# Kernel tuning notes

Hardware: AMD Instinct MI355X
Metric: run time of the kernel (lower is better)

The kernel has to match this reference:

```python
import jax, jax.numpy as jnp
import numpy as np

N_USERS = 100000
N_ITEMS = 50000
N_NODES = N_USERS + N_ITEMS
NNZ = 2400000
EMB_DIM = 64
N_LAYERS = 3
BATCH = 16384
REG = 1e-5


def setup_inputs() -> dict:
    key = jax.random.key(0)
    ks = jax.random.split(key, 12)
    return {
        "adj_row": jax.random.randint(ks[0], (NNZ,), 0, N_NODES, dtype=jnp.int32),
        "adj_col": jax.random.randint(ks[1], (NNZ,), 0, N_NODES, dtype=jnp.int32),
        "adj_val": jax.random.uniform(ks[2], (NNZ,), dtype=jnp.float32),
        "user_emb": jax.random.normal(ks[3], (N_USERS, EMB_DIM), dtype=jnp.float32) * 0.1,
        "item_emb": jax.random.normal(ks[4], (N_ITEMS, EMB_DIM), dtype=jnp.float32) * 0.1,
        "W1": jax.random.normal(ks[5], (N_LAYERS, EMB_DIM, EMB_DIM), dtype=jnp.float32) * 0.1,
        "b1": jax.random.normal(ks[6], (N_LAYERS, EMB_DIM), dtype=jnp.float32) * 0.1,
        "W2": jax.random.normal(ks[7], (N_LAYERS, EMB_DIM, EMB_DIM), dtype=jnp.float32) * 0.1,
        "b2": jax.random.normal(ks[8], (N_LAYERS, EMB_DIM), dtype=jnp.float32) * 0.1,
        "u": jax.random.randint(ks[9], (BATCH,), 0, N_USERS, dtype=jnp.int32),
        "i": jax.random.randint(ks[10], (BATCH,), 0, N_ITEMS, dtype=jnp.int32),
        "j": jax.random.randint(ks[11], (BATCH,), 0, N_ITEMS, dtype=jnp.int32),
    }


def _spmm(row, col, val, x):
    # sparse.mm(L, x): gather source rows, scale by edge value, scatter-add to dest
    msgs = val[:, None] * x[col]  # [nnz, d]
    return jax.ops.segment_sum(msgs, row, num_segments=N_NODES)


def reference(adj_row, adj_col, adj_val, user_emb, item_emb, W1, b1, W2, b2, u, i, j):
    ego = jnp.concatenate([user_emb, item_emb], axis=0)  # [N, d]
    finals = [ego]
    for k in range(N_LAYERS):
        side_L = _spmm(adj_row, adj_col, adj_val, ego)      # L @ ego
        side_LI = side_L + ego                               # (L + I) @ ego
        simple = side_LI @ W1[k] + b1[k]
        inter = (ego * side_L) @ W2[k] + b2[k]
        ego = jax.nn.leaky_relu(simple + inter, negative_slope=0.01)
        # mess_dropout = 0 -> identity; F.normalize(p=2, dim=1, eps=1e-12)
        nrm = jnp.linalg.norm(ego, axis=1, keepdims=True)
        finals.append(ego / jnp.maximum(nrm, 1e-12))
    final = jnp.concatenate(finals, axis=1)  # [N, d*(L+1)]
    u_f, i_f = final[:N_USERS], final[N_USERS:]
    u_emb = u_f[u]
    p_emb = i_f[i]
    n_emb = i_f[j]
    y_ui = jnp.sum(u_emb * p_emb, axis=1)
    y_uj = jnp.sum(u_emb * n_emb, axis=1)
    bpr_loss = -jnp.mean(jax.nn.log_sigmoid(y_ui - y_uj))
    l2norm = (jnp.sum(u_emb ** 2) / 2.0 + jnp.sum(p_emb ** 2) / 2.0 + jnp.sum(n_emb ** 2) / 2.0) / u_emb.shape[0]
    return bpr_loss + REG * l2norm
```

## Files before the change

kernel.cpp:

```cpp
#include <hip/hip_runtime.h>

#define N_USERS 100000
#define N_ITEMS 50000
#define N_NODES 150000
#define NNZ     2400000
#define EMB     64
#define NLAYERS 3
#define BATCH   16384
#define REG     1e-5f

#define NTILES ((N_NODES + 63) / 64)

#define ROWS_PER_BUCKET 256
#define NB_BUCKET ((N_NODES + ROWS_PER_BUCKET - 1) / ROWS_PER_BUCKET)
#define BIN_CHUNK 8192
#define BIN_NB ((NNZ + BIN_CHUNK - 1) / BIN_CHUNK)
#define BCAP 6144

#define F8_SCALE 16.0f
#define F8_INV   0.0625f

typedef __attribute__((ext_vector_type(8))) short bfrag8;
typedef __attribute__((ext_vector_type(4))) float vf4;
typedef __attribute__((ext_vector_type(2))) float f32x2;


__device__ inline unsigned short f2bf(float x) {
    unsigned int u = __builtin_bit_cast(unsigned int, x);
    return (unsigned short)((u + 0x7fffu + ((u >> 16) & 1u)) >> 16);
}
__device__ inline float bf2f(unsigned short h) {
    unsigned int u = ((unsigned int)h) << 16;
    return __builtin_bit_cast(float, u);
}

__global__ __launch_bounds__(256) void init_ego_kernel(
    const float* __restrict__ ue, const float* __restrict__ ie,
    unsigned short* __restrict__ ego_bf, unsigned char* __restrict__ ego_f8) {
    int idx = blockIdx.x * 256 + threadIdx.x;
    if (idx >= N_NODES * 16) return;
    int row = idx >> 4, q = idx & 15;
    const float* src = (row < N_USERS)
                           ? ue + (size_t)row * 64
                           : ie + (size_t)(row - N_USERS) * 64;
    float v0 = src[q], v1 = src[16 + q], v2 = src[32 + q], v3 = src[48 + q];
    uint2 o;
    o.x = (unsigned)f2bf(v0) | ((unsigned)f2bf(v1) << 16);
    o.y = (unsigned)f2bf(v2) | ((unsigned)f2bf(v3) << 16);
    ((uint2*)ego_bf)[(size_t)row * 16 + q] = o;
    int u = __builtin_amdgcn_cvt_pk_fp8_f32(v0 * F8_SCALE, v1 * F8_SCALE, 0,
                                            false);
    u = __builtin_amdgcn_cvt_pk_fp8_f32(v2 * F8_SCALE, v3 * F8_SCALE, u, true);
    ((int*)ego_f8)[(size_t)row * 16 + q] = u;
}

__global__ __launch_bounds__(256) void prep_w_kernel(
    const float* __restrict__ W1, const float* __restrict__ W2,
    unsigned short* __restrict__ BT) {
    int idx = blockIdx.x * blockDim.x + threadIdx.x;
    if (idx >= NLAYERS * 64 * 128) return;
    int l = idx / 8192;
    int rem = idx - l * 8192;
    int j = rem >> 7;
    int k = rem & 127;
    int p = k & 63;
    int d = ((p & 3) << 4) | (p >> 2);
    float w = (k < 64) ? W1[l * 4096 + d * 64 + j]
                       : W2[l * 4096 + d * 64 + j];
    BT[idx] = f2bf(w);
}

__global__ __launch_bounds__(1024) void binscatter_kernel(
    const int* __restrict__ row, const int* __restrict__ col,
    const float* __restrict__ val, int* __restrict__ bcnt,
    int2* __restrict__ stage) {
    __shared__ int hist[NB_BUCKET];
    __shared__ int wbase[NB_BUCKET];
    const int t = threadIdx.x;
    const int s = blockIdx.x * BIN_CHUNK;
    const int e = min(s + BIN_CHUNK, NNZ);

    for (int b = t; b < NB_BUCKET; b += 1024) hist[b] = 0;
    __syncthreads();
    for (int i = s + t; i < e; i += 1024)
        atomicAdd(&hist[row[i] >> 8], 1);
    __syncthreads();
    for (int b = t; b < NB_BUCKET; b += 1024) {
        int c = hist[b];
        wbase[b] = c ? atomicAdd(&bcnt[b], c) : 0;
        hist[b] = 0;
    }
    __syncthreads();
    for (int i0 = s + t; i0 < e; i0 += 4096) {
        int i1 = i0 + 1024, i2 = i0 + 2048, i3 = i0 + 3072;
        bool v1 = i1 < e, v2 = i2 < e, v3 = i3 < e;
        int r0 = row[i0];
        int r1 = v1 ? row[i1] : 0;
        int r2 = v2 ? row[i2] : 0;
        int r3 = v3 ? row[i3] : 0;
        int c0 = col[i0];
        int c1 = v1 ? col[i1] : 0;
        int c2 = v2 ? col[i2] : 0;
        int c3 = v3 ? col[i3] : 0;
        float w0 = val[i0];
        float w1 = v1 ? val[i1] : 0.f;
        float w2 = v2 ? val[i2] : 0.f;
        float w3 = v3 ? val[i3] : 0.f;
        int b0 = r0 >> 8, b1 = r1 >> 8, b2 = r2 >> 8, b3 = r3 >> 8;
        int o0 = atomicAdd(&hist[b0], 1);
        int o1 = v1 ? atomicAdd(&hist[b1], 1) : 0;
        int o2 = v2 ? atomicAdd(&hist[b2], 1) : 0;
        int o3 = v3 ? atomicAdd(&hist[b3], 1) : 0;
        stage[(size_t)b0 * BCAP + wbase[b0] + o0] =
            make_int2(c0 | ((r0 & 255) << 18), __builtin_bit_cast(int, w0));
        if (v1)
            stage[(size_t)b1 * BCAP + wbase[b1] + o1] =
                make_int2(c1 | ((r1 & 255) << 18), __builtin_bit_cast(int, w1));
        if (v2)
            stage[(size_t)b2 * BCAP + wbase[b2] + o2] =
                make_int2(c2 | ((r2 & 255) << 18), __builtin_bit_cast(int, w2));
        if (v3)
            stage[(size_t)b3 * BCAP + wbase[b3] + o3] =
                make_int2(c3 | ((r3 & 255) << 18), __builtin_bit_cast(int, w3));
    }
}

__global__ __launch_bounds__(1024) void bscan_kernel(
    const int* __restrict__ bcnt, int* __restrict__ bbase) {
    __shared__ int sc[1024];
    const int t = threadIdx.x;
    int v = (t < NB_BUCKET) ? bcnt[t] : 0;
    sc[t] = v;
    __syncthreads();
    int x = v;
    for (int off = 1; off < 1024; off <<= 1) {
        int y = (t >= off) ? sc[t - off] : 0;
        __syncthreads();
        x += y;
        sc[t] = x;
        __syncthreads();
    }
    if (t < NB_BUCKET) bbase[t] = x - v;
    if (t == 0) bbase[NB_BUCKET] = NNZ;
}

__global__ __launch_bounds__(1024) void bucket_place_kernel(
    const int2* __restrict__ stage, const int* __restrict__ bcnt,
    const int* __restrict__ bbase, int* __restrict__ rp,
    int2* __restrict__ sce) {
    __shared__ int cnt[ROWS_PER_BUCKET];
    __shared__ int sc[ROWS_PER_BUCKET];
    __shared__ int cur[ROWS_PER_BUCKET];
    const int b = blockIdx.x;
    const int t = threadIdx.x;
    const int row0 = b * ROWS_PER_BUCKET;
    const size_t S0 = (size_t)b * BCAP;
    const int ne = bcnt[b];
    const int B0 = bbase[b];
    if (t < 256) cnt[t] = 0;
    __syncthreads();
    for (int i = t; i < ne; i += 1024)
        atomicAdd(&cnt[(stage[S0 + i].x >> 18) & 255], 1);
    __syncthreads();
    int v = 0, x = 0;
    if (t < 256) { v = cnt[t]; x = v; sc[t] = v; }
    __syncthreads();
    for (int off = 1; off < 256; off <<= 1) {
        int y = (t < 256 && t >= off) ? sc[t - off] : 0;
        __syncthreads();
        if (t < 256) { x += y; sc[t] = x; }
        __syncthreads();
    }
    if (t < 256) {
        int excl = x - v;
        int row = row0 + t;
        if (row <= N_NODES) rp[row] = B0 + excl;
        cur[t] = B0 + excl;
    }
    __syncthreads();
    for (int i = t; i < ne; i += 1024) {
        int2 pk = stage[S0 + i];
        int rl = (pk.x >> 18) & 255;
        int pos = atomicAdd(&cur[rl], 1);
        sce[pos] = make_int2(pk.x & 0x3FFFF, pk.y);
    }
}

__global__ __launch_bounds__(256) void spmm_csr_kernel(
    const int* __restrict__ rp, const int2* __restrict__ sce,
    const unsigned char* __restrict__ ego_f8,
    unsigned short* __restrict__ side_bf) {
    const int lane = threadIdx.x & 63;
    const int q    = lane >> 4;
    const int ql   = lane & 15;
    int w = (blockIdx.x * blockDim.x + threadIdx.x) >> 6;
    int r0 = 2 * w;
    if (r0 >= N_NODES) return;
    int r1 = r0 + 1;
    const bool has1 = (r1 < N_NODES);
    const int* egoF = (const int*)ego_f8;
    int s0 = rp[r0];
    int e0 = rp[r0 + 1];
    int s1 = e0;
    int e1 = has1 ? rp[r0 + 2] : e0;
    float A0 = 0.f, A1 = 0.f, A2 = 0.f, A3 = 0.f;
    float B0 = 0.f, B1 = 0.f, B2 = 0.f, B3 = 0.f;

#define F8A(gi, wi)                                                          \
    {                                                                        \
        f32x2 lo_ = __builtin_amdgcn_cvt_pk_f32_fp8(gi, false);              \
        f32x2 hi_ = __builtin_amdgcn_cvt_pk_f32_fp8(gi, true);               \
        A0 = fmaf(wi, lo_.x, A0);                                            \
        A1 = fmaf(wi, lo_.y, A1);                                            \
        A2 = fmaf(wi, hi_.x, A2);                                            \
        A3 = fmaf(wi, hi_.y, A3);                                            \
    }
#define F8B(gi, wi)                                                          \
    {                                                                        \
        f32x2 lo_ = __builtin_amdgcn_cvt_pk_f32_fp8(gi, false);              \
        f32x2 hi_ = __builtin_amdgcn_cvt_pk_f32_fp8(gi, true);               \
        B0 = fmaf(wi, lo_.x, B0);                                            \
        B1 = fmaf(wi, lo_.y, B1);                                            \
        B2 = fmaf(wi, hi_.x, B2);                                            \
        B3 = fmaf(wi, hi_.y, B3);                                            \
    }

    int k0 = s0, k1 = s1;
    while (k0 + 15 < e0 || k1 + 15 < e1) {
        bool d0 = (k0 + 15 < e0), d1 = (k1 + 15 < e1);
        int2 cA0, cA1, cA2, cA3, cB0, cB1, cB2, cB3;
        int gA0 = 0, gA1 = 0, gA2 = 0, gA3 = 0;
        int gB0 = 0, gB1 = 0, gB2 = 0, gB3 = 0;
        if (d0) {
            cA0 = sce[k0 + q];      cA1 = sce[k0 + 4 + q];
            cA2 = sce[k0 + 8 + q];  cA3 = sce[k0 + 12 + q];
        }
        if (d1) {
            cB0 = sce[k1 + q];      cB1 = sce[k1 + 4 + q];
            cB2 = sce[k1 + 8 + q];  cB3 = sce[k1 + 12 + q];
        }
        if (d0) {
            gA0 = egoF[(size_t)cA0.x * 16 + ql];
            gA1 = egoF[(size_t)cA1.x * 16 + ql];
            gA2 = egoF[(size_t)cA2.x * 16 + ql];
            gA3 = egoF[(size_t)cA3.x * 16 + ql];
        }
        if (d1) {
            gB0 = egoF[(size_t)cB0.x * 16 + ql];
            gB1 = egoF[(size_t)cB1.x * 16 + ql];
            gB2 = egoF[(size_t)cB2.x * 16 + ql];
            gB3 = egoF[(size_t)cB3.x * 16 + ql];
        }
        if (d0) {
            F8A(gA0, __builtin_bit_cast(float, cA0.y))
            F8A(gA1, __builtin_bit_cast(float, cA1.y))
            F8A(gA2, __builtin_bit_cast(float, cA2.y))
            F8A(gA3, __builtin_bit_cast(float, cA3.y))
            k0 += 16;
        }
        if (d1) {
            F8B(gB0, __builtin_bit_cast(float, cB0.y))
            F8B(gB1, __builtin_bit_cast(float, cB1.y))
            F8B(gB2, __builtin_bit_cast(float, cB2.y))
            F8B(gB3, __builtin_bit_cast(float, cB3.y))
            k1 += 16;
        }
    }
    {
        bool t0 = (k0 < e0), t1 = (k1 < e1);
        int2 cA0, cA1, cA2, cA3, cB0, cB1, cB2, cB3;
        int gA0 = 0, gA1 = 0, gA2 = 0, gA3 = 0;
        int gB0 = 0, gB1 = 0, gB2 = 0, gB3 = 0;
        if (t0) {
            int la = e0 - 1;
            cA0 = sce[min(k0 + q, la)];      cA1 = sce[min(k0 + 4 + q, la)];
            cA2 = sce[min(k0 + 8 + q, la)];  cA3 = sce[min(k0 + 12 + q, la)];
        }
        if (t1) {
            int lb = e1 - 1;
            cB0 = sce[min(k1 + q, lb)];      cB1 = sce[min(k1 + 4 + q, lb)];
            cB2 = sce[min(k1 + 8 + q, lb)];  cB3 = sce[min(k1 + 12 + q, lb)];
        }
        if (t0) {
            gA0 = egoF[(size_t)cA0.x * 16 + ql];
            gA1 = egoF[(size_t)cA1.x * 16 + ql];
            gA2 = egoF[(size_t)cA2.x * 16 + ql];
            gA3 = egoF[(size_t)cA3.x * 16 + ql];
        }
        if (t1) {
            gB0 = egoF[(size_t)cB0.x * 16 + ql];
            gB1 = egoF[(size_t)cB1.x * 16 + ql];
            gB2 = egoF[(size_t)cB2.x * 16 + ql];
            gB3 = egoF[(size_t)cB3.x * 16 + ql];
        }
        if (t0) {
            float w0 = (k0 + q      < e0) ? __builtin_bit_cast(float, cA0.y) : 0.f;
            float w1 = (k0 + 4 + q  < e0) ? __builtin_bit_cast(float, cA1.y) : 0.f;
            float w2 = (k0 + 8 + q  < e0) ? __builtin_bit_cast(float, cA2.y) : 0.f;
            float w3 = (k0 + 12 + q < e0) ? __builtin_bit_cast(float, cA3.y) : 0.f;
            F8A(gA0, w0) F8A(gA1, w1) F8A(gA2, w2) F8A(gA3, w3)
        }
        if (t1) {
            float w0 = (k1 + q      < e1) ? __builtin_bit_cast(float, cB0.y) : 0.f;
            float w1 = (k1 + 4 + q  < e1) ? __builtin_bit_cast(float, cB1.y) : 0.f;
            float w2 = (k1 + 8 + q  < e1) ? __builtin_bit_cast(float, cB2.y) : 0.f;
            float w3 = (k1 + 12 + q < e1) ? __builtin_bit_cast(float, cB3.y) : 0.f;
            F8B(gB0, w0) F8B(gB1, w1) F8B(gB2, w2) F8B(gB3, w3)
        }
    }
#undef F8A
#undef F8B
    A0 += __shfl_xor(A0, 32, 64); A0 += __shfl_xor(A0, 16, 64);
    A1 += __shfl_xor(A1, 32, 64); A1 += __shfl_xor(A1, 16, 64);
    A2 += __shfl_xor(A2, 32, 64); A2 += __shfl_xor(A2, 16, 64);
    A3 += __shfl_xor(A3, 32, 64); A3 += __shfl_xor(A3, 16, 64);
    B0 += __shfl_xor(B0, 32, 64); B0 += __shfl_xor(B0, 16, 64);
    B1 += __shfl_xor(B1, 32, 64); B1 += __shfl_xor(B1, 16, 64);
    B2 += __shfl_xor(B2, 32, 64); B2 += __shfl_xor(B2, 16, 64);
    B3 += __shfl_xor(B3, 32, 64); B3 += __shfl_xor(B3, 16, 64);
    if (q == 0) {
        uint2 oA;
        oA.x = (unsigned)f2bf(A0 * F8_INV) | ((unsigned)f2bf(A1 * F8_INV) << 16);
        oA.y = (unsigned)f2bf(A2 * F8_INV) | ((unsigned)f2bf(A3 * F8_INV) << 16);
        ((uint2*)side_bf)[(size_t)r0 * 16 + ql] = oA;
        if (has1) {
            uint2 oB;
            oB.x = (unsigned)f2bf(B0 * F8_INV) |
                   ((unsigned)f2bf(B1 * F8_INV) << 16);
            oB.y = (unsigned)f2bf(B2 * F8_INV) |
                   ((unsigned)f2bf(B3 * F8_INV) << 16);
            ((uint2*)side_bf)[(size_t)r1 * 16 + ql] = oB;
        }
    }
}

__global__ __launch_bounds__(256) void gemm_dense_kernel(
    unsigned short* __restrict__ ego,
    unsigned char* __restrict__ ego_f8,
    const unsigned short* __restrict__ side_bf,
    const unsigned short* __restrict__ BT, const float* __restrict__ b1,
    const float* __restrict__ b2, float* __restrict__ nrm) {
    __shared__ unsigned short A_lds[64][136];
    const int tid  = threadIdx.x;
    const int lane = tid & 63, wm = tid >> 6;
    const int m = lane & 15, g = lane >> 4;
    const int base = blockIdx.x * 64;

    bfrag8 b[4][4];
#pragma unroll
    for (int nt = 0; nt < 4; ++nt)
#pragma unroll
        for (int kt = 0; kt < 4; ++kt)
            b[nt][kt] =
                *(const bfrag8*)(BT + (nt * 16 + m) * 128 + kt * 32 + g * 8);

    float bias[4];
#pragma unroll
    for (int nt = 0; nt < 4; ++nt)
        bias[nt] = b1[nt * 16 + m] + b2[nt * 16 + m];

#pragma unroll
    for (int it = 0; it < 2; ++it) {
        int idx = it * 256 + tid;
        int n = idx >> 3, c = idx & 7;
        int node = base + n;
        uint4 ev = make_uint4(0, 0, 0, 0), sv = make_uint4(0, 0, 0, 0);
        if (node < N_NODES) {
            ev = ((const uint4*)ego)[(size_t)node * 8 + c];
            sv = ((const uint4*)side_bf)[(size_t)node * 8 + c];
        }
        unsigned evu[4] = {ev.x, ev.y, ev.z, ev.w};
        unsigned svu[4] = {sv.x, sv.y, sv.z, sv.w};
        unsigned qv[4], pq[4];
#pragma unroll
        for (int j = 0; j < 4; ++j) {
            float e0 = bf2f((unsigned short)(evu[j] & 0xffffu));
            float e1 = bf2f((unsigned short)(evu[j] >> 16));
            float s0 = bf2f((unsigned short)(svu[j] & 0xffffu));
            float s1 = bf2f((unsigned short)(svu[j] >> 16));
            qv[j] = f2bf(e0 + s0) | ((unsigned)f2bf(e1 + s1) << 16);
            pq[j] = f2bf(e0 * s0) | ((unsigned)f2bf(e1 * s1) << 16);
        }
        *(uint4*)&A_lds[n][c * 8]      = make_uint4(qv[0], qv[1], qv[2], qv[3]);
        *(uint4*)&A_lds[n][64 + c * 8] = make_uint4(pq[0], pq[1], pq[2], pq[3]);
    }
    __syncthreads();

    bfrag8 a[4];
#pragma unroll
    for (int kt = 0; kt < 4; ++kt)
        a[kt] = *(const bfrag8*)&A_lds[wm * 16 + m][kt * 32 + g * 8];

    vf4 acc[4];
#pragma unroll
    for (int nt = 0; nt < 4; ++nt) acc[nt] = (vf4){0.f, 0.f, 0.f, 0.f};
#pragma unroll
    for (int kt = 0; kt < 4; ++kt)
#pragma unroll
        for (int nt = 0; nt < 4; ++nt)
            acc[nt] = __builtin_amdgcn_mfma_f32_16x16x32_bf16(
                a[kt], b[nt][kt], acc[nt], 0, 0, 0);

    float o[4][4];
    float sq[4] = {0.f, 0.f, 0.f, 0.f};
#pragma unroll
    for (int nt = 0; nt < 4; ++nt)
#pragma unroll
        for (int r = 0; r < 4; ++r) {
            float v = acc[nt][r] + bias[nt];
            v = (v >= 0.f) ? v : 0.01f * v;
            o[nt][r] = v;
            sq[r] += v * v;
        }
#pragma unroll
    for (int r = 0; r < 4; ++r)
#pragma unroll
        for (int off = 1; off < 16; off <<= 1)
            sq[r] += __shfl_xor(sq[r], off, 64);

#pragma unroll
    for (int r = 0; r < 4; ++r) {
        int row = base + wm * 16 + g * 4 + r;
        if (row < N_NODES) {
            uint2 ob;
            ob.x = (unsigned)f2bf(o[0][r]) | ((unsigned)f2bf(o[1][r]) << 16);
            ob.y = (unsigned)f2bf(o[2][r]) | ((unsigned)f2bf(o[3][r]) << 16);
            ((uint2*)ego)[(size_t)row * 16 + m] = ob;
            int uf = __builtin_amdgcn_cvt_pk_fp8_f32(
                o[0][r] * F8_SCALE, o[1][r] * F8_SCALE, 0, false);
            uf = __builtin_amdgcn_cvt_pk_fp8_f32(
                o[2][r] * F8_SCALE, o[3][r] * F8_SCALE, uf, true);
            ((int*)ego_f8)[(size_t)row * 16 + m] = uf;
            if (m == 0) nrm[row] = fmaxf(sqrtf(sq[r]), 1e-12f);
        }
    }
}

__global__ __launch_bounds__(256) void batch_kernel(
    const unsigned short* __restrict__ ego_bf, const float* __restrict__ nrm,
    int use_nrm, const int* __restrict__ u, const int* __restrict__ pi,
    const int* __restrict__ ni, float* __restrict__ dot_ui,
    float* __restrict__ dot_uj, float* __restrict__ l2b) {
    const int lane = threadIdx.x & 63;
    int b = (blockIdx.x * blockDim.x + threadIdx.x) >> 6;
    if (b >= BATCH) return;
    int un = u[b];
    int pn = N_USERS + pi[b];
    int nn = N_USERS + ni[b];
    float fu = bf2f(ego_bf[(size_t)un * EMB + lane]);
    float fp = bf2f(ego_bf[(size_t)pn * EMB + lane]);
    float fn_ = bf2f(ego_bf[(size_t)nn * EMB + lane]);
    if (use_nrm) {
        fu /= nrm[un];
        fp /= nrm[pn];
        fn_ /= nrm[nn];
    }
    float dup = fu * fp;
    float dun = fu * fn_;
    float l2  = fu * fu + fp * fp + fn_ * fn_;
#pragma unroll
    for (int off = 32; off; off >>= 1) {
        dup += __shfl_xor(dup, off, 64);
        dun += __shfl_xor(dun, off, 64);
        l2  += __shfl_xor(l2, off, 64);
    }
    if (lane == 0) {
        dot_ui[b] += dup;
        dot_uj[b] += dun;
        l2b[b]    += l2;
    }
}

__global__ __launch_bounds__(256) void loss_partial_kernel(
    const float* __restrict__ dot_ui, const float* __restrict__ dot_uj,
    const float* __restrict__ l2b, float* __restrict__ partial) {
    __shared__ float sl[256], s2[256];
    const int t = threadIdx.x;
    const int b = blockIdx.x * 256 + t;
    float x = dot_ui[b] - dot_uj[b];
    float sp = (x > 0.f) ? log1pf(expf(-x)) : (-x + log1pf(expf(x)));
    sl[t] = sp;
    s2[t] = l2b[b];
    __syncthreads();
    for (int off = 128; off; off >>= 1) {
        if (t < off) {
            sl[t] += sl[t + off];
            s2[t] += s2[t + off];
        }
        __syncthreads();
    }
    if (t == 0) {
        partial[blockIdx.x]      = sl[0];
        partial[64 + blockIdx.x] = s2[0];
    }
}

__global__ void loss_final_kernel(const float* __restrict__ partial,
                                  float* __restrict__ out) {
    const int t = threadIdx.x;
    float sp = partial[t];
    float l2 = partial[64 + t];
#pragma unroll
    for (int off = 32; off; off >>= 1) {
        sp += __shfl_down(sp, off, 64);
        l2 += __shfl_down(l2, off, 64);
    }
    if (t == 0)
        out[0] = sp / (float)BATCH + REG * (l2 * 0.5f / (float)BATCH);
}

extern "C" void kernel_launch(void* const* d_in, const int* in_sizes, int n_in,
                              void* d_out, int out_size, void* d_ws,
                              size_t ws_size, hipStream_t stream) {
    const int*   adj_row  = (const int*)d_in[0];
    const int*   adj_col  = (const int*)d_in[1];
    const float* adj_val  = (const float*)d_in[2];
    const float* user_emb = (const float*)d_in[3];
    const float* item_emb = (const float*)d_in[4];
    const float* W1       = (const float*)d_in[5];
    const float* b1       = (const float*)d_in[6];
    const float* W2       = (const float*)d_in[7];
    const float* b2       = (const float*)d_in[8];
    const int*   u        = (const int*)d_in[9];
    const int*   ii       = (const int*)d_in[10];
    const int*   jj       = (const int*)d_in[11];

    char* p = (char*)d_ws;
    auto alloc = [&](size_t bytes) {
        char* q = p;
        p += (bytes + 255) & ~(size_t)255;
        return q;
    };
    unsigned short* ego    = (unsigned short*)alloc((size_t)N_NODES * EMB * 2);
    unsigned char*  ego_f8 = (unsigned char*)alloc((size_t)N_NODES * EMB);
    unsigned short* side_bf= (unsigned short*)alloc((size_t)N_NODES * EMB * 2);
    int2*           sce    = (int2*)alloc((size_t)NNZ * 8);
    int2*           stage  = (int2*)alloc((size_t)NB_BUCKET * BCAP * 8);
    int*            rp     = (int*)alloc((size_t)(N_NODES + 1) * 4);
    int*            bcnt   = (int*)alloc((size_t)NB_BUCKET * 4);
    int*            bbase  = (int*)alloc((size_t)(NB_BUCKET + 1) * 4);
    float*          nrm    = (float*)alloc((size_t)N_NODES * 4);
    float*          dot_ui = (float*)alloc((size_t)BATCH * 4);
    float*          dot_uj = (float*)alloc((size_t)BATCH * 4);
    float*          l2b    = (float*)alloc((size_t)BATCH * 4);
    float*          partial= (float*)alloc(128 * 4);
    unsigned short* BT     = (unsigned short*)alloc((size_t)NLAYERS * 8192 * 2);

    hipMemsetAsync(dot_ui, 0, BATCH * sizeof(float), stream);
    hipMemsetAsync(dot_uj, 0, BATCH * sizeof(float), stream);
    hipMemsetAsync(l2b, 0, BATCH * sizeof(float), stream);
    hipMemsetAsync(bcnt, 0, NB_BUCKET * sizeof(int), stream);

    prep_w_kernel<<<(NLAYERS * 8192 + 255) / 256, 256, 0, stream>>>(W1, W2, BT);

    binscatter_kernel<<<BIN_NB, 1024, 0, stream>>>(adj_row, adj_col, adj_val,
                                                   bcnt, stage);
    bscan_kernel<<<1, 1024, 0, stream>>>(bcnt, bbase);
    bucket_place_kernel<<<NB_BUCKET, 1024, 0, stream>>>(stage, bcnt, bbase, rp,
                                                        sce);

    init_ego_kernel<<<(N_NODES * 16 + 255) / 256, 256, 0, stream>>>(
        user_emb, item_emb, ego, ego_f8);

    batch_kernel<<<BATCH / 4, 256, 0, stream>>>(ego, nrm, 0, u, ii, jj,
                                                dot_ui, dot_uj, l2b);

    const int spmm_blocks = ((N_NODES + 1) / 2 * 64 + 255) / 256;
    for (int k = 0; k < NLAYERS; ++k) {
        spmm_csr_kernel<<<spmm_blocks, 256, 0, stream>>>(rp, sce, ego_f8,
                                                         side_bf);
        gemm_dense_kernel<<<NTILES, 256, 0, stream>>>(
            ego, ego_f8, side_bf, BT + (size_t)k * 8192, b1 + (size_t)k * EMB,
            b2 + (size_t)k * EMB, nrm);
        batch_kernel<<<BATCH / 4, 256, 0, stream>>>(ego, nrm, 1, u, ii, jj,
                                                    dot_ui, dot_uj, l2b);
    }

    loss_partial_kernel<<<BATCH / 256, 256, 0, stream>>>(dot_ui, dot_uj, l2b,
                                                         partial);
    loss_final_kernel<<<1, 64, 0, stream>>>(partial, (float*)d_out);
}
```

Baseline: 328.6 us.

## Widen SpMM gathers to 8-byte loads and double CSR bucket size

The SpMM kernel now has each group of 8 lanes fetch a full fp8 embedding row with 8-byte loads, instead of 16 lanes using 4-byte loads. Each lane keeps 8 accumulators, the shuffle reduction adds one step, and outputs are written with 16-byte stores. This cuts gather instruction count and sce loads per edge. Separately, the binning used to build the CSR now uses 512-row buckets with a larger staging capacity, halving the bucket count. The trade-offs are a bigger staging buffer and longer per-bucket scans, plus higher register pressure in SpMM.

```diff
diff --git a/kernel.cpp b/kernel.cpp
--- a/kernel.cpp
+++ b/kernel.cpp
@@ -11,11 +11,11 @@
 
 #define NTILES ((N_NODES + 63) / 64)
 
-#define ROWS_PER_BUCKET 256
+#define ROWS_PER_BUCKET 512
 #define NB_BUCKET ((N_NODES + ROWS_PER_BUCKET - 1) / ROWS_PER_BUCKET)
 #define BIN_CHUNK 8192
 #define BIN_NB ((NNZ + BIN_CHUNK - 1) / BIN_CHUNK)
-#define BCAP 6144
+#define BCAP 10240
 
 #define F8_SCALE 16.0f
 #define F8_INV   0.0625f
@@ -80,15 +80,15 @@
     const int s = blockIdx.x * BIN_CHUNK;
     const int e = min(s + BIN_CHUNK, NNZ);
 
-    for (int b = t; b < NB_BUCKET; b += 1024) hist[b] = 0;
+    if (t < NB_BUCKET) hist[t] = 0;
     __syncthreads();
     for (int i = s + t; i < e; i += 1024)
-        atomicAdd(&hist[row[i] >> 8], 1);
-    __syncthreads();
-    for (int b = t; b < NB_BUCKET; b += 1024) {
-        int c = hist[b];
-        wbase[b] = c ? atomicAdd(&bcnt[b], c) : 0;
-        hist[b] = 0;
+        atomicAdd(&hist[row[i] >> 9], 1);
+    __syncthreads();
+    if (t < NB_BUCKET) {
+        int c = hist[t];
+        wbase[t] = c ? atomicAdd(&bcnt[t], c) : 0;
+        hist[t] = 0;
     }
     __syncthreads();
     for (int i0 = s + t; i0 < e; i0 += 4096) {
@@ -106,22 +106,22 @@
         float w1 = v1 ? val[i1] : 0.f;
         float w2 = v2 ? val[i2] : 0.f;
         float w3 = v3 ? val[i3] : 0.f;
-        int b0 = r0 >> 8, b1 = r1 >> 8, b2 = r2 >> 8, b3 = r3 >> 8;
+        int b0 = r0 >> 9, b1 = r1 >> 9, b2 = r2 >> 9, b3 = r3 >> 9;
         int o0 = atomicAdd(&hist[b0], 1);
         int o1 = v1 ? atomicAdd(&hist[b1], 1) : 0;
         int o2 = v2 ? atomicAdd(&hist[b2], 1) : 0;
         int o3 = v3 ? atomicAdd(&hist[b3], 1) : 0;
         stage[(size_t)b0 * BCAP + wbase[b0] + o0] =
-            make_int2(c0 | ((r0 & 255) << 18), __builtin_bit_cast(int, w0));
+            make_int2(c0 | ((r0 & 511) << 18), __builtin_bit_cast(int, w0));
         if (v1)
             stage[(size_t)b1 * BCAP + wbase[b1] + o1] =
-                make_int2(c1 | ((r1 & 255) << 18), __builtin_bit_cast(int, w1));
+                make_int2(c1 | ((r1 & 511) << 18), __builtin_bit_cast(int, w1));
         if (v2)
             stage[(size_t)b2 * BCAP + wbase[b2] + o2] =
-                make_int2(c2 | ((r2 & 255) << 18), __builtin_bit_cast(int, w2));
+                make_int2(c2 | ((r2 & 511) << 18), __builtin_bit_cast(int, w2));
         if (v3)
             stage[(size_t)b3 * BCAP + wbase[b3] + o3] =
-                make_int2(c3 | ((r3 & 255) << 18), __builtin_bit_cast(int, w3));
+                make_int2(c3 | ((r3 & 511) << 18), __builtin_bit_cast(int, w3));
     }
 }
 
@@ -157,21 +157,21 @@
     const size_t S0 = (size_t)b * BCAP;
     const int ne = bcnt[b];
     const int B0 = bbase[b];
-    if (t < 256) cnt[t] = 0;
+    if (t < ROWS_PER_BUCKET) cnt[t] = 0;
     __syncthreads();
     for (int i = t; i < ne; i += 1024)
-        atomicAdd(&cnt[(stage[S0 + i].x >> 18) & 255], 1);
+        atomicAdd(&cnt[(stage[S0 + i].x >> 18) & 511], 1);
     __syncthreads();
     int v = 0, x = 0;
-    if (t < 256) { v = cnt[t]; x = v; sc[t] = v; }
-    __syncthreads();
-    for (int off = 1; off < 256; off <<= 1) {
-        int y = (t < 256 && t >= off) ? sc[t - off] : 0;
+    if (t < ROWS_PER_BUCKET) { v = cnt[t]; x = v; sc[t] = v; }
+    __syncthreads();
+    for (int off = 1; off < ROWS_PER_BUCKET; off <<= 1) {
+        int y = (t < ROWS_PER_BUCKET && t >= off) ? sc[t - off] : 0;
         __syncthreads();
-        if (t < 256) { x += y; sc[t] = x; }
+        if (t < ROWS_PER_BUCKET) { x += y; sc[t] = x; }
         __syncthreads();
     }
-    if (t < 256) {
+    if (t < ROWS_PER_BUCKET) {
         int excl = x - v;
         int row = row0 + t;
         if (row <= N_NODES) rp[row] = B0 + excl;
@@ -180,7 +180,7 @@
     __syncthreads();
     for (int i = t; i < ne; i += 1024) {
         int2 pk = stage[S0 + i];
-        int rl = (pk.x >> 18) & 255;
+        int rl = (pk.x >> 18) & 511;
         int pos = atomicAdd(&cur[rl], 1);
         sce[pos] = make_int2(pk.x & 0x3FFFF, pk.y);
     }
@@ -191,145 +191,132 @@
     const unsigned char* __restrict__ ego_f8,
     unsigned short* __restrict__ side_bf) {
     const int lane = threadIdx.x & 63;
-    const int q    = lane >> 4;
-    const int ql   = lane & 15;
+    const int g8 = lane >> 3;
+    const int ol = lane & 7;
     int w = (blockIdx.x * blockDim.x + threadIdx.x) >> 6;
     int r0 = 2 * w;
     if (r0 >= N_NODES) return;
     int r1 = r0 + 1;
     const bool has1 = (r1 < N_NODES);
-    const int* egoF = (const int*)ego_f8;
+    const uint2* egoV = (const uint2*)ego_f8;
     int s0 = rp[r0];
     int e0 = rp[r0 + 1];
-    int s1 = e0;
     int e1 = has1 ? rp[r0 + 2] : e0;
     float A0 = 0.f, A1 = 0.f, A2 = 0.f, A3 = 0.f;
+    float A4 = 0.f, A5 = 0.f, A6 = 0.f, A7 = 0.f;
     float B0 = 0.f, B1 = 0.f, B2 = 0.f, B3 = 0.f;
-
-#define F8A(gi, wi)                                                          \
+    float B4 = 0.f, B5 = 0.f, B6 = 0.f, B7 = 0.f;
+
+#define DECA(gv, wt)                                                         \
     {                                                                        \
-        f32x2 lo_ = __builtin_amdgcn_cvt_pk_f32_fp8(gi, false);              \
-        f32x2 hi_ = __builtin_amdgcn_cvt_pk_f32_fp8(gi, true);               \
-        A0 = fmaf(wi, lo_.x, A0);                                            \
-        A1 = fmaf(wi, lo_.y, A1);                                            \
-        A2 = fmaf(wi, hi_.x, A2);                                            \
-        A3 = fmaf(wi, hi_.y, A3);                                            \
-    }
-#define F8B(gi, wi)                                                          \
+        f32x2 p0 = __builtin_amdgcn_cvt_pk_f32_fp8((gv).x, false);           \
+        f32x2 p1 = __builtin_amdgcn_cvt_pk_f32_fp8((gv).x, true);            \
+        f32x2 p2 = __builtin_amdgcn_cvt_pk_f32_fp8((gv).y, false);           \
+        f32x2 p3 = __builtin_amdgcn_cvt_pk_f32_fp8((gv).y, true);            \
+        A0 = fmaf(wt, p0.x, A0); A1 = fmaf(wt, p0.y, A1);                    \
+        A2 = fmaf(wt, p1.x, A2); A3 = fmaf(wt, p1.y, A3);                    \
+        A4 = fmaf(wt, p2.x, A4); A5 = fmaf(wt, p2.y, A5);                    \
+        A6 = fmaf(wt, p3.x, A6); A7 = fmaf(wt, p3.y, A7);                    \
+    }
+#define DECB(gv, wt)                                                         \
     {                                                                        \
-        f32x2 lo_ = __builtin_amdgcn_cvt_pk_f32_fp8(gi, false);              \
-        f32x2 hi_ = __builtin_amdgcn_cvt_pk_f32_fp8(gi, true);               \
-        B0 = fmaf(wi, lo_.x, B0);                                            \
-        B1 = fmaf(wi, lo_.y, B1);                                            \
-        B2 = fmaf(wi, hi_.x, B2);                                            \
-        B3 = fmaf(wi, hi_.y, B3);                                            \
-    }
-
-    int k0 = s0, k1 = s1;
+        f32x2 p0 = __builtin_amdgcn_cvt_pk_f32_fp8((gv).x, false);           \
+        f32x2 p1 = __builtin_amdgcn_cvt_pk_f32_fp8((gv).x, true);            \
+        f32x2 p2 = __builtin_amdgcn_cvt_pk_f32_fp8((gv).y, false);           \
+        f32x2 p3 = __builtin_amdgcn_cvt_pk_f32_fp8((gv).y, true);            \
+        B0 = fmaf(wt, p0.x, B0); B1 = fmaf(wt, p0.y, B1);                    \
+        B2 = fmaf(wt, p1.x, B2); B3 = fmaf(wt, p1.y, B3);                    \
+        B4 = fmaf(wt, p2.x, B4); B5 = fmaf(wt, p2.y, B5);                    \
+        B6 = fmaf(wt, p3.x, B6); B7 = fmaf(wt, p3.y, B7);                    \
+    }
+
+    int k0 = s0, k1 = e0;
     while (k0 + 15 < e0 || k1 + 15 < e1) {
         bool d0 = (k0 + 15 < e0), d1 = (k1 + 15 < e1);
-        int2 cA0, cA1, cA2, cA3, cB0, cB1, cB2, cB3;
-        int gA0 = 0, gA1 = 0, gA2 = 0, gA3 = 0;
-        int gB0 = 0, gB1 = 0, gB2 = 0, gB3 = 0;
+        int2 cA0, cA1, cB0, cB1;
+        uint2 gA0, gA1, gB0, gB1;
+        if (d0) { cA0 = sce[k0 + g8]; cA1 = sce[k0 + 8 + g8]; }
+        if (d1) { cB0 = sce[k1 + g8]; cB1 = sce[k1 + 8 + g8]; }
         if (d0) {
-            cA0 = sce[k0 + q];      cA1 = sce[k0 + 4 + q];
-            cA2 = sce[k0 + 8 + q];  cA3 = sce[k0 + 12 + q];
+            gA0 = egoV[(size_t)cA0.x * 8 + ol];
+            gA1 = egoV[(size_t)cA1.x * 8 + ol];
         }
         if (d1) {
-            cB0 = sce[k1 + q];      cB1 = sce[k1 + 4 + q];
-            cB2 = sce[k1 + 8 + q];  cB3 = sce[k1 + 12 + q];
+            gB0 = egoV[(size_t)cB0.x * 8 + ol];
+            gB1 = egoV[(size_t)cB1.x * 8 + ol];
         }
         if (d0) {
-            gA0 = egoF[(size_t)cA0.x * 16 + ql];
-            gA1 = egoF[(size_t)cA1.x * 16 + ql];
-            gA2 = egoF[(size_t)cA2.x * 16 + ql];
-            gA3 = egoF[(size_t)cA3.x * 16 + ql];
+            DECA(gA0, __builtin_bit_cast(float, cA0.y))
+            DECA(gA1, __builtin_bit_cast(float, cA1.y))
+            k0 += 16;
         }
         if (d1) {
-            gB0 = egoF[(size_t)cB0.x * 16 + ql];
-            gB1 = egoF[(size_t)cB1.x * 16 + ql];
-            gB2 = egoF[(size_t)cB2.x * 16 + ql];
-            gB3 = egoF[(size_t)cB3.x * 16 + ql];
-        }
-        if (d0) {
-            F8A(gA0, __builtin_bit_cast(float, cA0.y))
-            F8A(gA1, __builtin_bit_cast(float, cA1.y))
-            F8A(gA2, __builtin_bit_cast(float, cA2.y))
-            F8A(gA3, __builtin_bit_cast(float, cA3.y))
-            k0 += 16;
-        }
-        if (d1) {
-            F8B(gB0, __builtin_bit_cast(float, cB0.y))
-            F8B(gB1, __builtin_bit_cast(float, cB1.y))
-            F8B(gB2, __builtin_bit_cast(float, cB2.y))
-            F8B(gB3, __builtin_bit_cast(float, cB3.y))
+            DECB(gB0, __builtin_bit_cast(float, cB0.y))
+            DECB(gB1, __builtin_bit_cast(float, cB1.y))
             k1 += 16;
         }
     }
     {
         bool t0 = (k0 < e0), t1 = (k1 < e1);
-        int2 cA0, cA1, cA2, cA3, cB0, cB1, cB2, cB3;
-        int gA0 = 0, gA1 = 0, gA2 = 0, gA3 = 0;
-        int gB0 = 0, gB1 = 0, gB2 = 0, gB3 = 0;
+        int2 cA0, cA1, cB0, cB1;
+        uint2 gA0, gA1, gB0, gB1;
         if (t0) {
             int la = e0 - 1;
-            cA0 = sce[min(k0 + q, la)];      cA1 = sce[min(k0 + 4 + q, la)];
-            cA2 = sce[min(k0 + 8 + q, la)];  cA3 = sce[min(k0 + 12 + q, la)];
+            cA0 = sce[min(k0 + g8, la)];
+            cA1 = sce[min(k0 + 8 + g8, la)];
         }
         if (t1) {
             int lb = e1 - 1;
-            cB0 = sce[min(k1 + q, lb)];      cB1 = sce[min(k1 + 4 + q, lb)];
-            cB2 = sce[min(k1 + 8 + q, lb)];  cB3 = sce[min(k1 + 12 + q, lb)];
+            cB0 = sce[min(k1 + g8, lb)];
+            cB1 = sce[min(k1 + 8 + g8, lb)];
         }
         if (t0) {
-            gA0 = egoF[(size_t)cA0.x * 16 + ql];
-            gA1 = egoF[(size_t)cA1.x * 16 + ql];
-            gA2 = egoF[(size_t)cA2.x * 16 + ql];
-            gA3 = egoF[(size_t)cA3.x * 16 + ql];
+            gA0 = egoV[(size_t)cA0.x * 8 + ol];
+            gA1 = egoV[(size_t)cA1.x * 8 + ol];
         }
         if (t1) {
-            gB0 = egoF[(size_t)cB0.x * 16 + ql];
-            gB1 = egoF[(size_t)cB1.x * 16 + ql];
-            gB2 = egoF[(size_t)cB2.x * 16 + ql];
-            gB3 = egoF[(size_t)cB3.x * 16 + ql];
+            gB0 = egoV[(size_t)cB0.x * 8 + ol];
+            gB1 = egoV[(size_t)cB1.x * 8 + ol];
         }
         if (t0) {
-            float w0 = (k0 + q      < e0) ? __builtin_bit_cast(float, cA0.y) : 0.f;
-            float w1 = (k0 + 4 + q  < e0) ? __builtin_bit_cast(float, cA1.y) : 0.f;
-            float w2 = (k0 + 8 + q  < e0) ? __builtin_bit_cast(float, cA2.y) : 0.f;
-            float w3 = (k0 + 12 + q < e0) ? __builtin_bit_cast(float, cA3.y) : 0.f;
-            F8A(gA0, w0) F8A(gA1, w1) F8A(gA2, w2) F8A(gA3, w3)
+            float w0 = (k0 + g8 < e0) ? __builtin_bit_cast(float, cA0.y) : 0.f;
+            float w1 =
+                (k0 + 8 + g8 < e0) ? __builtin_bit_cast(float, cA1.y) : 0.f;
+            DECA(gA0, w0) DECA(gA1, w1)
         }
         if (t1) {
-            float w0 = (k1 + q      < e1) ? __builtin_bit_cast(float, cB0.y) : 0.f;
-            float w1 = (k1 + 4 + q  < e1) ? __builtin_bit_cast(float, cB1.y) : 0.f;
-            float w2 = (k1 + 8 + q  < e1) ? __builtin_bit_cast(float, cB2.y) : 0.f;
-            float w3 = (k1 + 12 + q < e1) ? __builtin_bit_cast(float, cB3.y) : 0.f;
-            F8B(gB0, w0) F8B(gB1, w1) F8B(gB2, w2) F8B(gB3, w3)
-        }
-    }
-#undef F8A
-#undef F8B
-    A0 += __shfl_xor(A0, 32, 64); A0 += __shfl_xor(A0, 16, 64);
-    A1 += __shfl_xor(A1, 32, 64); A1 += __shfl_xor(A1, 16, 64);
-    A2 += __shfl_xor(A2, 32, 64); A2 += __shfl_xor(A2, 16, 64);
-    A3 += __shfl_xor(A3, 32, 64); A3 += __shfl_xor(A3, 16, 64);
-    B0 += __shfl_xor(B0, 32, 64); B0 += __shfl_xor(B0, 16, 64);
-    B1 += __shfl_xor(B1, 32, 64); B1 += __shfl_xor(B1, 16, 64);
-    B2 += __shfl_xor(B2, 32, 64); B2 += __shfl_xor(B2, 16, 64);
-    B3 += __shfl_xor(B3, 32, 64); B3 += __shfl_xor(B3, 16, 64);
-    if (q == 0) {
-        uint2 oA;
+            float w0 = (k1 + g8 < e1) ? __builtin_bit_cast(float, cB0.y) : 0.f;
+            float w1 =
+                (k1 + 8 + g8 < e1) ? __builtin_bit_cast(float, cB1.y) : 0.f;
+            DECB(gB0, w0) DECB(gB1, w1)
+        }
+    }
+#undef DECA
+#undef DECB
+#define RED(a)                                                               \
+    a += __shfl_xor(a, 32, 64); a += __shfl_xor(a, 16, 64);                  \
+    a += __shfl_xor(a, 8, 64);
+    RED(A0) RED(A1) RED(A2) RED(A3) RED(A4) RED(A5) RED(A6) RED(A7)
+    RED(B0) RED(B1) RED(B2) RED(B3) RED(B4) RED(B5) RED(B6) RED(B7)
+#undef RED
+    if (g8 == 0) {
+        uint4 oA;
         oA.x = (unsigned)f2bf(A0 * F8_INV) | ((unsigned)f2bf(A1 * F8_INV) << 16);
         oA.y = (unsigned)f2bf(A2 * F8_INV) | ((unsigned)f2bf(A3 * F8_INV) << 16);
-        ((uint2*)side_bf)[(size_t)r0 * 16 + ql] = oA;
+        oA.z = (unsigned)f2bf(A4 * F8_INV) | ((unsigned)f2bf(A5 * F8_INV) << 16);
+        oA.w = (unsigned)f2bf(A6 * F8_INV) | ((unsigned)f2bf(A7 * F8_INV) << 16);
+        ((uint4*)side_bf)[(size_t)r0 * 8 + ol] = oA;
         if (has1) {
-            uint2 oB;
+            uint4 oB;
             oB.x = (unsigned)f2bf(B0 * F8_INV) |
                    ((unsigned)f2bf(B1 * F8_INV) << 16);
             oB.y = (unsigned)f2bf(B2 * F8_INV) |
                    ((unsigned)f2bf(B3 * F8_INV) << 16);
-            ((uint2*)side_bf)[(size_t)r1 * 16 + ql] = oB;
+            oB.z = (unsigned)f2bf(B4 * F8_INV) |
+                   ((unsigned)f2bf(B5 * F8_INV) << 16);
+            oB.w = (unsigned)f2bf(B6 * F8_INV) |
+                   ((unsigned)f2bf(B7 * F8_INV) << 16);
+            ((uint4*)side_bf)[(size_t)r1 * 8 + ol] = oB;
         }
     }
 }
```

Result: slower. 341.4 us (+3.9%).
